# Kernel tuning notes

Hardware: AMD Instinct MI355X
Metric: run time of the kernel (lower is better)

The kernel has to match this reference:

```python
import jax, jax.numpy as jnp
import numpy as np

HEADS = 8
DIM_HEAD = 64
BN_EPS = 1e-5

def setup_inputs() -> dict:
    key = jax.random.key(0)
    ks = jax.random.split(key, 6)
    B, N, D = 8, 1024, 512
    inner = HEADS * DIM_HEAD  # 512
    return {
        "x": jax.random.normal(ks[0], (B, N, D), dtype=jnp.float32),
        "w_qkv": jax.random.normal(ks[1], (D, 3 * inner), dtype=jnp.float32) * (D ** -0.5),
        "conv_w": jax.random.normal(ks[2], (HEADS, HEADS), dtype=jnp.float32) * (HEADS ** -0.5),
        "conv_b": jax.random.normal(ks[3], (HEADS,), dtype=jnp.float32) * 0.02,
        "bn_gamma": jnp.ones((HEADS,), dtype=jnp.float32),
        "bn_beta": jnp.zeros((HEADS,), dtype=jnp.float32),
        "w_out": jax.random.normal(ks[4], (inner, D), dtype=jnp.float32) * (inner ** -0.5),
        "b_out": jnp.zeros((D,), dtype=jnp.float32),
    }

def reference(x, w_qkv, conv_w, conv_b, bn_gamma, bn_beta, w_out, b_out):
    B, N, D = x.shape
    H, dh = HEADS, DIM_HEAD
    scale = dh ** -0.5
    qkv = x @ w_qkv  # [B, N, 3*H*dh]
    q, k, v = jnp.split(qkv, 3, axis=-1)
    # b n (h d) -> b h n d
    q = q.reshape(B, N, H, dh).transpose(0, 2, 1, 3)
    k = k.reshape(B, N, H, dh).transpose(0, 2, 1, 3)
    v = v.reshape(B, N, H, dh).transpose(0, 2, 1, 3)
    attn = jnp.einsum('bhnd,bhmd->bhnm', q, k) * scale
    attn = jax.nn.softmax(attn, axis=-1)
    # 1x1 conv across heads (channels = heads)
    attn = jnp.einsum('gh,bhnm->bgnm', conv_w, attn) + conv_b[None, :, None, None]
    # BatchNorm2d in training mode: batch stats over (B, N, N) per head, biased variance
    mean = attn.mean(axis=(0, 2, 3), keepdims=True)
    var = attn.var(axis=(0, 2, 3), keepdims=True)
    attn = (attn - mean) * jax.lax.rsqrt(var + BN_EPS)
    attn = attn * bn_gamma[None, :, None, None] + bn_beta[None, :, None, None]
    # reatten_scale = 1.0 (transform_scale=False)
    out = jnp.einsum('bhnm,bhmd->bhnd', attn, v)
    out = out.transpose(0, 2, 1, 3).reshape(B, N, H * dh)  # b h n d -> b n (h d)
    return out @ w_out + b_out
```

## Files before the change

kernel.cpp:

```cpp
#include <hip/hip_runtime.h>
#include <math.h>


#define Bz 8
#define Nn 1024
#define Dd 512
#define Hh 8
#define DH 64
#define INNER 512
#define QW 1536
#define SCALE 0.125f
#define BN_EPS 1e-5f

typedef short bf16x8 __attribute__((ext_vector_type(8)));
typedef float f32x4 __attribute__((ext_vector_type(4)));

#define MFMA(a, b, c) __builtin_amdgcn_mfma_f32_16x16x32_bf16((a), (b), (c), 0, 0, 0)

__device__ __forceinline__ unsigned short f2b(float f) {
  union { float f; unsigned u; } v; v.f = f;
  unsigned r = v.u + 0x7fffu + ((v.u >> 16) & 1u);
  return (unsigned short)(r >> 16);
}
__device__ __forceinline__ float b2f(unsigned short s) {
  union { unsigned u; float f; } v; v.u = ((unsigned)s) << 16;
  return v.f;
}

#define WB_XB 0u
#define WB_QKV 8388608u
#define WB_O1A 0u
#define WB_O1B 16777216u
#define WB_VT 33554432u
#define WB_SG 41943040u
#define WB_O1BF WB_SG
#define WB_WQT 176160768u
#define WB_WOT 177733632u
#define WB_RSUM 178257920u
#define WB_VSUM 178520064u
#define WB_STATS 178536448u
#define WB_AC 178536512u

__global__ __launch_bounds__(256) void k_xbf(const float* __restrict__ X,
                                             unsigned short* __restrict__ XB) {
  const size_t i = ((size_t)blockIdx.x * 256 + threadIdx.x) * 8;
  float4 f0 = *(const float4*)(X + i);
  float4 f1 = *(const float4*)(X + i + 4);
  unsigned short o[8] = {f2b(f0.x), f2b(f0.y), f2b(f0.z), f2b(f0.w),
                         f2b(f1.x), f2b(f1.y), f2b(f1.z), f2b(f1.w)};
  *(uint4*)(XB + i) = *(uint4*)o;
}

__global__ __launch_bounds__(256) void k_transpose(const float* __restrict__ src,
                                                   unsigned short* __restrict__ dst,
                                                   int R, int C) {
  __shared__ float tile[32][33];
  const int tc = blockIdx.x * 32, tr = blockIdx.y * 32;
  const int lx = threadIdx.x & 31, ly = threadIdx.x >> 5;
#pragma unroll
  for (int i = 0; i < 32; i += 8)
    tile[ly + i][lx] = src[(size_t)(tr + ly + i) * C + tc + lx];
  __syncthreads();
#pragma unroll
  for (int i = 0; i < 32; i += 8)
    dst[(size_t)(tc + ly + i) * R + tr + lx] = f2b(tile[lx][ly + i]);
}

__global__ __launch_bounds__(256) void k_qkv(const unsigned short* __restrict__ XB,
                                             const unsigned short* __restrict__ WQT,
                                             unsigned short* __restrict__ qkv,
                                             unsigned short* __restrict__ vT) {
  extern __shared__ char smem[];
  unsigned short(*sA)[40] = (unsigned short(*)[40])smem;
  unsigned short(*sB)[40] = (unsigned short(*)[40])(smem + 128 * 40 * 2);
  unsigned short* sEp = (unsigned short*)smem;
  const int t = threadIdx.x;
  const int col0 = blockIdx.x * 128;
  const int row0 = blockIdx.y * 128;
  const bool isqk = (col0 < 2 * INNER);
  const int l = t & 63, w = t >> 6;
  const int wm = (w & 1) * 64, wn = (w >> 1) * 64;
  const int lm = l & 15, lq = l >> 4;
  const int srow = t >> 1, skc = (t & 1) * 16;
  f32x4 acc[4][4] = {};
  for (int k0 = 0; k0 < Dd; k0 += 32) {
    {
      const unsigned short* src = XB + (size_t)(row0 + srow) * Dd + k0 + skc;
      *(uint4*)&sA[srow][skc] = *(const uint4*)src;
      *(uint4*)&sA[srow][skc + 8] = *(const uint4*)(src + 8);
    }
    {
      const unsigned short* srcB = WQT + (size_t)(col0 + srow) * Dd + k0 + skc;
      *(uint4*)&sB[srow][skc] = *(const uint4*)srcB;
      *(uint4*)&sB[srow][skc + 8] = *(const uint4*)(srcB + 8);
    }
    __syncthreads();
    bf16x8 af[4], bfr[4];
#pragma unroll
    for (int i = 0; i < 4; i++) af[i] = *(const bf16x8*)&sA[wm + 16 * i + lm][lq * 8];
#pragma unroll
    for (int j = 0; j < 4; j++) bfr[j] = *(const bf16x8*)&sB[wn + 16 * j + lm][lq * 8];
    if (isqk) {
#pragma unroll
      for (int i = 0; i < 4; i++)
#pragma unroll
        for (int j = 0; j < 4; j++) acc[i][j] = MFMA(bfr[i], af[j], acc[i][j]);
    } else {
#pragma unroll
      for (int i = 0; i < 4; i++)
#pragma unroll
        for (int j = 0; j < 4; j++) acc[i][j] = MFMA(af[i], bfr[j], acc[i][j]);
    }
    __syncthreads();
  }
  if (isqk) {
#pragma unroll
    for (int jc = 0; jc < 4; jc++)
#pragma unroll
      for (int ir = 0; ir < 4; ir++) {
        unsigned short us[4];
#pragma unroll
        for (int r = 0; r < 4; r++) us[r] = f2b(acc[jc][ir][r]);
        *(uint2*)&sEp[(wm + 16 * ir + lm) * 136 + wn + 16 * jc + 4 * lq] = *(uint2*)us;
      }
    __syncthreads();
    const int row = t >> 1, half = t & 1;
    const unsigned short* src = &sEp[row * 136 + half * 64];
    unsigned short* dst = qkv + (size_t)(row0 + row) * QW + col0 + half * 64;
#pragma unroll
    for (int c = 0; c < 8; c++) *(uint4*)(dst + c * 8) = *(const uint4*)(src + c * 8);
  } else {
#pragma unroll
    for (int ir = 0; ir < 4; ir++)
#pragma unroll
      for (int jc = 0; jc < 4; jc++) {
        unsigned short us[4];
#pragma unroll
        for (int r = 0; r < 4; r++) us[r] = f2b(acc[ir][jc][r]);
        *(uint2*)&sEp[(wn + 16 * jc + lm) * 136 + wm + 16 * ir + 4 * lq] = *(uint2*)us;
      }
    __syncthreads();
    const int row = t >> 1, half = t & 1;
    const int gd = col0 - 2 * INNER + row;
    const int bq = row0 >> 10, mseq0 = row0 & 1023;
    const unsigned short* src = &sEp[row * 136 + half * 64];
    unsigned short* dst =
        vT + (((size_t)(bq * Hh + (gd >> 6)) * DH + (gd & 63)) << 10) + mseq0 + half * 64;
#pragma unroll
    for (int c = 0; c < 8; c++) *(uint4*)(dst + c * 8) = *(const uint4*)(src + c * 8);
  }
}

__global__ __launch_bounds__(256) void k_vsum(const unsigned short* __restrict__ vT,
                                              float* __restrict__ vsum) {
  const int bg = blockIdx.x;
  const int d = threadIdx.x >> 2, qq = threadIdx.x & 3;
  __shared__ float red[64][4];
  const unsigned short* p = vT + ((size_t)bg * DH + d) * Nn + qq * 256;
  float s = 0.f;
  for (int m = 0; m < 256; m += 4) {
    uint2 rr = *(const uint2*)(p + m);
    s += b2f((unsigned short)(rr.x & 0xffff)) + b2f((unsigned short)(rr.x >> 16)) +
         b2f((unsigned short)(rr.y & 0xffff)) + b2f((unsigned short)(rr.y >> 16));
  }
  red[d][qq] = s;
  __syncthreads();
  if (threadIdx.x < 64)
    vsum[(size_t)bg * DH + threadIdx.x] =
        red[threadIdx.x][0] + red[threadIdx.x][1] + red[threadIdx.x][2] + red[threadIdx.x][3];
}

__global__ __launch_bounds__(512, 4) void k_sgen(const unsigned short* __restrict__ qkv,
                                                 unsigned short* __restrict__ Sg,
                                                 float* __restrict__ rsum) {
  __shared__ unsigned short sK[8 * 32 * 72];
  __shared__ unsigned short sT[32 * 264];
  const int b = blockIdx.x;
  const int n0 = blockIdx.y * 32;
  const int mh = blockIdx.z;
  const int t = threadIdx.x;
  const int w = t >> 6, l = t & 63;
  const int lm = l & 15, lq = l >> 4;
  bf16x8 qf[2][2];
#pragma unroll
  for (int i = 0; i < 2; i++) {
    const unsigned short* qp =
        qkv + (size_t)(b * Nn + n0 + 16 * i + lm) * QW + w * DH + lq * 8;
    qf[i][0] = *(const bf16x8*)qp;
    qf[i][1] = *(const bf16x8*)(qp + 32);
  }
  float psum[2] = {0.f, 0.f};
  for (int it = 0; it < 16; it++) {
    const int m0 = mh * 512 + it * 32;
    {
#pragma unroll
      for (int s = 0; s < 4; s++) {
        const int c = t + s * 512;
        const int hh = c >> 8, mm = (c >> 3) & 31, qq = c & 7;
        *(uint4*)&sK[(hh * 32 + mm) * 72 + qq * 8] = *(const uint4*)(
            qkv + (size_t)(b * Nn + m0 + mm) * QW + INNER + hh * DH + qq * 8);
      }
    }
    __syncthreads();
    f32x4 lac[2][2] = {};
#pragma unroll
    for (int jm = 0; jm < 2; jm++) {
      bf16x8 ka0 = *(const bf16x8*)&sK[(w * 32 + 16 * jm + lm) * 72 + lq * 8];
      bf16x8 ka1 = *(const bf16x8*)&sK[(w * 32 + 16 * jm + lm) * 72 + 32 + lq * 8];
#pragma unroll
      for (int i = 0; i < 2; i++) {
        lac[i][jm] = MFMA(ka0, qf[i][0], lac[i][jm]);
        lac[i][jm] = MFMA(ka1, qf[i][1], lac[i][jm]);
      }
    }
#pragma unroll
    for (int i = 0; i < 2; i++)
#pragma unroll
      for (int jm = 0; jm < 2; jm++)
#pragma unroll
        for (int r = 0; r < 4; r++) {
          float e = __expf(lac[i][jm][r] * SCALE);
          psum[i] += e;
          sT[(16 * i + lm) * 264 + (16 * jm + 4 * lq + r) * 8 + w] = f2b(e);
        }
    __syncthreads();
    {
      const int row = t >> 4, ck = t & 15;
      unsigned short* dst =
          Sg + (((size_t)(b * Nn + n0 + row) << 10) + m0) * 8 + ck * 16;
      const unsigned short* src = &sT[row * 264 + ck * 16];
      *(uint4*)dst = *(const uint4*)src;
      *(uint4*)(dst + 8) = *(const uint4*)(src + 8);
    }
  }
#pragma unroll
  for (int i = 0; i < 2; i++) {
    psum[i] += __shfl_xor(psum[i], 16);
    psum[i] += __shfl_xor(psum[i], 32);
  }
  if (lq == 0) {
    atomicAdd(&rsum[(size_t)(b * Hh + w) * Nn + n0 + lm], psum[0]);
    atomicAdd(&rsum[(size_t)(b * Hh + w) * Nn + n0 + 16 + lm], psum[1]);
  }
}

__global__ __launch_bounds__(512, 4) void k_mixsv(const unsigned short* __restrict__ Sg,
                                                  const unsigned short* __restrict__ vT,
                                                  const float* __restrict__ rsum,
                                                  const float* __restrict__ conv_w,
                                                  float* __restrict__ O1A,
                                                  float* __restrict__ O1B,
                                                  float* __restrict__ stats) {
  __shared__ unsigned short sU[2][8][16][68];
  __shared__ float sRed[8][16];
  const int b = blockIdx.x;
  const int n0 = blockIdx.y * 16;
  const int mbase = blockIdx.z * 512;
  float* __restrict__ O1 = blockIdx.z ? O1B : O1A;
  const int t = threadIdx.x;
  const int w = t >> 6, l = t & 63;
  const int lm = l & 15, lq = l >> 4;
  const int mxn = t >> 5, mxm = (t & 31) * 2;
  float cw[64];
#pragma unroll
  for (int i = 0; i < 64; i++) cw[i] = conv_w[i];
  float rv[8];
#pragma unroll
  for (int h = 0; h < 8; h++) rv[h] = 1.0f / rsum[(size_t)(b * Hh + h) * Nn + n0 + mxn];
  const unsigned short* sN = Sg + ((size_t)(b * Nn + n0 + mxn) << 13);
  f32x4 oacc[4] = {};
  float su[8] = {}, su2[8] = {};
  uint4 sreg[2][2];
  {
    const unsigned short* p = sN + ((size_t)(mbase + mxm) << 3);
    sreg[0][0] = *(const uint4*)p;
    sreg[0][1] = *(const uint4*)(p + 8);
  }
#pragma unroll
  for (int it = 0; it < 8; it++) {
    const int cur = it & 1, nxt = cur ^ 1;
    if (it < 7) {
      const unsigned short* p = sN + ((size_t)(mbase + (it + 1) * 64 + mxm) << 3);
      sreg[nxt][0] = *(const uint4*)p;
      sreg[nxt][1] = *(const uint4*)(p + 8);
    }
    {
      float sx[8], sy[8];
      const unsigned* pe = (const unsigned*)&sreg[cur][0];
      const unsigned* po = (const unsigned*)&sreg[cur][1];
#pragma unroll
      for (int h = 0; h < 4; h++) {
        sx[2 * h] = b2f((unsigned short)(pe[h] & 0xffff)) * rv[2 * h];
        sx[2 * h + 1] = b2f((unsigned short)(pe[h] >> 16)) * rv[2 * h + 1];
        sy[2 * h] = b2f((unsigned short)(po[h] & 0xffff)) * rv[2 * h];
        sy[2 * h + 1] = b2f((unsigned short)(po[h] >> 16)) * rv[2 * h + 1];
      }
#pragma unroll
      for (int g = 0; g < 8; g++) {
        float u0 = 0.f, u1 = 0.f;
#pragma unroll
        for (int h = 0; h < 8; h++) {
          u0 += cw[g * 8 + h] * sx[h];
          u1 += cw[g * 8 + h] * sy[h];
        }
        su[g] += u0 + u1;
        su2[g] += u0 * u0 + u1 * u1;
        *(unsigned*)&sU[cur][g][mxn][mxm] = (unsigned)f2b(u0) | ((unsigned)f2b(u1) << 16);
      }
    }
    __syncthreads();
    {
      bf16x8 uf0 = *(const bf16x8*)&sU[cur][w][lm][lq * 8];
      bf16x8 uf1 = *(const bf16x8*)&sU[cur][w][lm][32 + lq * 8];
#pragma unroll
      for (int j = 0; j < 4; j++) {
        const unsigned short* vp =
            vT + (((size_t)(b * Hh + w) * DH + 16 * j + lm) << 10) + mbase + it * 64 + lq * 8;
        bf16x8 v0 = *(const bf16x8*)vp;
        bf16x8 v1 = *(const bf16x8*)(vp + 32);
        oacc[j] = MFMA(uf0, v0, oacc[j]);
        oacc[j] = MFMA(uf1, v1, oacc[j]);
      }
    }
  }
#pragma unroll
  for (int j = 0; j < 4; j++)
#pragma unroll
    for (int r = 0; r < 4; r++)
      O1[((size_t)(b * Hh + w) * Nn + n0 + lq * 4 + r) * DH + 16 * j + lm] = oacc[j][r];
#pragma unroll
  for (int g = 0; g < 8; g++) {
    float a = su[g], q = su2[g];
    for (int off = 32; off; off >>= 1) {
      a += __shfl_down(a, off);
      q += __shfl_down(q, off);
    }
    if (l == 0) {
      sRed[w][g] = a;
      sRed[w][8 + g] = q;
    }
  }
  __syncthreads();
  if (t < 16) {
    float s = 0.f;
#pragma unroll
    for (int ww = 0; ww < 8; ww++) s += sRed[ww][t];
    atomicAdd(&stats[t], s);
  }
}

__global__ void k_alpha(const float* __restrict__ stats, const float* __restrict__ bn_gamma,
                        const float* __restrict__ bn_beta, float* __restrict__ ac) {
  const int g = threadIdx.x;
  if (g < 8) {
    const float cnt = (float)Bz * (float)Nn * (float)Nn;
    float Eu = stats[g] / cnt;
    float Eu2 = stats[8 + g] / cnt;
    float inv = rsqrtf(Eu2 - Eu * Eu + BN_EPS);
    float alpha = bn_gamma[g] * inv;
    ac[g] = alpha;
    ac[8 + g] = bn_beta[g] - Eu * alpha;
  }
}

__global__ __launch_bounds__(256) void k_o1aff(const float* __restrict__ O1A,
                                               const float* __restrict__ O1B,
                                               const float* __restrict__ vsum,
                                               const float* __restrict__ ac,
                                               unsigned short* __restrict__ O1BF) {
  const size_t i4 = ((size_t)blockIdx.x * 256 + threadIdx.x) * 4;
  const int bg = (int)(i4 >> 16);
  const int g = bg & 7;
  const int d = (int)(i4 & 63);
  float4 a = *(const float4*)(O1A + i4);
  float4 bb = *(const float4*)(O1B + i4);
  float4 v = *(const float4*)(vsum + (size_t)bg * DH + d);
  const float al = ac[g], cc = ac[8 + g];
  unsigned short o[4] = {f2b(al * (a.x + bb.x) + cc * v.x), f2b(al * (a.y + bb.y) + cc * v.y),
                         f2b(al * (a.z + bb.z) + cc * v.z), f2b(al * (a.w + bb.w) + cc * v.w)};
  *(uint2*)(O1BF + i4) = *(uint2*)o;
}

__global__ __launch_bounds__(256) void k_out(const unsigned short* __restrict__ O1BF,
                                             const unsigned short* __restrict__ WOT,
                                             const float* __restrict__ bout,
                                             float* __restrict__ out) {
  __shared__ unsigned short sA[128][40];
  __shared__ unsigned short sB[128][40];
  const int t = threadIdx.x;
  const int col0 = blockIdx.x * 128, row0 = blockIdx.y * 128;
  const int l = t & 63, w = t >> 6;
  const int wm = (w & 1) * 64, wn = (w >> 1) * 64;
  const int lm = l & 15, lq = l >> 4;
  const int srow = t >> 1, skc = (t & 1) * 16;
  const int b = row0 >> 10;
  const int nn = (row0 + srow) & 1023;
  f32x4 acc[4][4] = {};
  for (int k0 = 0; k0 < INNER; k0 += 32) {
    {
      const int k = k0 + skc;
      const int g = k >> 6, dd = k & 63;
      const unsigned short* src = O1BF + ((size_t)(b * Hh + g) * Nn + nn) * DH + dd;
      *(uint4*)&sA[srow][skc] = *(const uint4*)src;
      *(uint4*)&sA[srow][skc + 8] = *(const uint4*)(src + 8);
    }
    {
      const unsigned short* srcB = WOT + (size_t)(col0 + srow) * INNER + k0 + skc;
      *(uint4*)&sB[srow][skc] = *(const uint4*)srcB;
      *(uint4*)&sB[srow][skc + 8] = *(const uint4*)(srcB + 8);
    }
    __syncthreads();
    bf16x8 af[4], bfr[4];
#pragma unroll
    for (int i = 0; i < 4; i++) af[i] = *(const bf16x8*)&sA[wm + 16 * i + lm][lq * 8];
#pragma unroll
    for (int j = 0; j < 4; j++) bfr[j] = *(const bf16x8*)&sB[wn + 16 * j + lm][lq * 8];
#pragma unroll
    for (int i = 0; i < 4; i++)
#pragma unroll
      for (int j = 0; j < 4; j++) acc[i][j] = MFMA(af[i], bfr[j], acc[i][j]);
    __syncthreads();
  }
#pragma unroll
  for (int j = 0; j < 4; j++) {
    const int col = col0 + wn + 16 * j + lm;
    const float bo = bout[col];
#pragma unroll
    for (int i = 0; i < 4; i++) {
      const int rbase = row0 + wm + 16 * i + lq * 4;
#pragma unroll
      for (int r = 0; r < 4; r++) out[(size_t)(rbase + r) * Dd + col] = acc[i][j][r] + bo;
    }
  }
}

extern "C" void kernel_launch(void* const* d_in, const int* in_sizes, int n_in,
                              void* d_out, int out_size, void* d_ws, size_t ws_size,
                              hipStream_t stream) {
  const float* x = (const float*)d_in[0];
  const float* w_qkv = (const float*)d_in[1];
  const float* conv_w = (const float*)d_in[2];
  const float* bn_gamma = (const float*)d_in[4];
  const float* bn_beta = (const float*)d_in[5];
  const float* w_out = (const float*)d_in[6];
  const float* b_out = (const float*)d_in[7];
  char* ws = (char*)d_ws;
  unsigned short* XB = (unsigned short*)(ws + WB_XB);
  unsigned short* QKV = (unsigned short*)(ws + WB_QKV);
  unsigned short* VT = (unsigned short*)(ws + WB_VT);
  unsigned short* SG = (unsigned short*)(ws + WB_SG);
  unsigned short* WQT = (unsigned short*)(ws + WB_WQT);
  unsigned short* WOT = (unsigned short*)(ws + WB_WOT);
  float* O1Ap = (float*)(ws + WB_O1A);
  float* O1Bp = (float*)(ws + WB_O1B);
  unsigned short* O1BF = (unsigned short*)(ws + WB_O1BF);
  float* RSUM = (float*)(ws + WB_RSUM);
  float* VSUM = (float*)(ws + WB_VSUM);
  float* STATS = (float*)(ws + WB_STATS);
  float* AC = (float*)(ws + WB_AC);

  hipMemsetAsync(STATS, 0, 64, stream);
  hipMemsetAsync(RSUM, 0, 262144, stream);
  k_xbf<<<2048, 256, 0, stream>>>(x, XB);
  k_transpose<<<dim3(48, 16), 256, 0, stream>>>(w_qkv, WQT, 512, 1536);
  k_transpose<<<dim3(16, 16), 256, 0, stream>>>(w_out, WOT, 512, 512);
  k_qkv<<<dim3(12, 64), 256, 34816, stream>>>(XB, WQT, QKV, VT);
  k_vsum<<<64, 256, 0, stream>>>(VT, VSUM);
  k_sgen<<<dim3(8, 32, 2), 512, 0, stream>>>(QKV, SG, RSUM);
  k_mixsv<<<dim3(8, 64, 2), 512, 0, stream>>>(SG, VT, RSUM, conv_w, O1Ap, O1Bp, STATS);
  k_alpha<<<1, 64, 0, stream>>>(STATS, bn_gamma, bn_beta, AC);
  k_o1aff<<<4096, 256, 0, stream>>>(O1Ap, O1Bp, VSUM, AC, O1BF);
  k_out<<<dim3(4, 64), 256, 0, stream>>>(O1BF, WOT, b_out, (float*)d_out);
}
```

Baseline: 328.4 us.

## Switch bf16 to fp16 MFMA and merge split-M mixsv into one pass

```diff
diff --git a/kernel.cpp b/kernel.cpp
--- a/kernel.cpp
+++ b/kernel.cpp
@@ -12,25 +12,26 @@
 #define SCALE 0.125f
 #define BN_EPS 1e-5f
 
-typedef short bf16x8 __attribute__((ext_vector_type(8)));
+typedef _Float16 __f16;
+typedef __f16 f16x8 __attribute__((ext_vector_type(8)));
 typedef float f32x4 __attribute__((ext_vector_type(4)));
 
-#define MFMA(a, b, c) __builtin_amdgcn_mfma_f32_16x16x32_bf16((a), (b), (c), 0, 0, 0)
-
-__device__ __forceinline__ unsigned short f2b(float f) {
-  union { float f; unsigned u; } v; v.f = f;
-  unsigned r = v.u + 0x7fffu + ((v.u >> 16) & 1u);
-  return (unsigned short)(r >> 16);
-}
-__device__ __forceinline__ float b2f(unsigned short s) {
-  union { unsigned u; float f; } v; v.u = ((unsigned)s) << 16;
-  return v.f;
+#define MFMA16(a, b, c) __builtin_amdgcn_mfma_f32_16x16x32_f16((a), (b), (c), 0, 0, 0)
+
+__device__ __forceinline__ unsigned short f2h(float f) {
+  union { __f16 h; unsigned short s; } v;
+  v.h = (__f16)f;
+  return v.s;
+}
+__device__ __forceinline__ float h2f(unsigned short s) {
+  union { unsigned short s; __f16 h; } v;
+  v.s = s;
+  return (float)v.h;
 }
 
 #define WB_XB 0u
 #define WB_QKV 8388608u
-#define WB_O1A 0u
-#define WB_O1B 16777216u
+#define WB_O1 0u
 #define WB_VT 33554432u
 #define WB_SG 41943040u
 #define WB_O1BF WB_SG
@@ -46,8 +47,8 @@
   const size_t i = ((size_t)blockIdx.x * 256 + threadIdx.x) * 8;
   float4 f0 = *(const float4*)(X + i);
   float4 f1 = *(const float4*)(X + i + 4);
-  unsigned short o[8] = {f2b(f0.x), f2b(f0.y), f2b(f0.z), f2b(f0.w),
-                         f2b(f1.x), f2b(f1.y), f2b(f1.z), f2b(f1.w)};
+  unsigned short o[8] = {f2h(f0.x), f2h(f0.y), f2h(f0.z), f2h(f0.w),
+                         f2h(f1.x), f2h(f1.y), f2h(f1.z), f2h(f1.w)};
   *(uint4*)(XB + i) = *(uint4*)o;
 }
 
@@ -63,7 +64,7 @@
   __syncthreads();
 #pragma unroll
   for (int i = 0; i < 32; i += 8)
-    dst[(size_t)(tc + ly + i) * R + tr + lx] = f2b(tile[lx][ly + i]);
+    dst[(size_t)(tc + ly + i) * R + tr + lx] = f2h(tile[lx][ly + i]);
 }
 
 __global__ __launch_bounds__(256) void k_qkv(const unsigned short* __restrict__ XB,
@@ -95,21 +96,21 @@
       *(uint4*)&sB[srow][skc + 8] = *(const uint4*)(srcB + 8);
     }
     __syncthreads();
-    bf16x8 af[4], bfr[4];
-#pragma unroll
-    for (int i = 0; i < 4; i++) af[i] = *(const bf16x8*)&sA[wm + 16 * i + lm][lq * 8];
-#pragma unroll
-    for (int j = 0; j < 4; j++) bfr[j] = *(const bf16x8*)&sB[wn + 16 * j + lm][lq * 8];
+    f16x8 af[4], bfr[4];
+#pragma unroll
+    for (int i = 0; i < 4; i++) af[i] = *(const f16x8*)&sA[wm + 16 * i + lm][lq * 8];
+#pragma unroll
+    for (int j = 0; j < 4; j++) bfr[j] = *(const f16x8*)&sB[wn + 16 * j + lm][lq * 8];
     if (isqk) {
 #pragma unroll
       for (int i = 0; i < 4; i++)
 #pragma unroll
-        for (int j = 0; j < 4; j++) acc[i][j] = MFMA(bfr[i], af[j], acc[i][j]);
+        for (int j = 0; j < 4; j++) acc[i][j] = MFMA16(bfr[i], af[j], acc[i][j]);
     } else {
 #pragma unroll
       for (int i = 0; i < 4; i++)
 #pragma unroll
-        for (int j = 0; j < 4; j++) acc[i][j] = MFMA(af[i], bfr[j], acc[i][j]);
+        for (int j = 0; j < 4; j++) acc[i][j] = MFMA16(af[i], bfr[j], acc[i][j]);
     }
     __syncthreads();
   }
@@ -120,7 +121,7 @@
       for (int ir = 0; ir < 4; ir++) {
         unsigned short us[4];
 #pragma unroll
-        for (int r = 0; r < 4; r++) us[r] = f2b(acc[jc][ir][r]);
+        for (int r = 0; r < 4; r++) us[r] = f2h(acc[jc][ir][r]);
         *(uint2*)&sEp[(wm + 16 * ir + lm) * 136 + wn + 16 * jc + 4 * lq] = *(uint2*)us;
       }
     __syncthreads();
@@ -136,7 +137,7 @@
       for (int jc = 0; jc < 4; jc++) {
         unsigned short us[4];
 #pragma unroll
-        for (int r = 0; r < 4; r++) us[r] = f2b(acc[ir][jc][r]);
+        for (int r = 0; r < 4; r++) us[r] = f2h(acc[ir][jc][r]);
         *(uint2*)&sEp[(wn + 16 * jc + lm) * 136 + wm + 16 * ir + 4 * lq] = *(uint2*)us;
       }
     __syncthreads();
@@ -160,8 +161,8 @@
   float s = 0.f;
   for (int m = 0; m < 256; m += 4) {
     uint2 rr = *(const uint2*)(p + m);
-    s += b2f((unsigned short)(rr.x & 0xffff)) + b2f((unsigned short)(rr.x >> 16)) +
-         b2f((unsigned short)(rr.y & 0xffff)) + b2f((unsigned short)(rr.y >> 16));
+    s += h2f((unsigned short)(rr.x & 0xffff)) + h2f((unsigned short)(rr.x >> 16)) +
+         h2f((unsigned short)(rr.y & 0xffff)) + h2f((unsigned short)(rr.y >> 16));
   }
   red[d][qq] = s;
   __syncthreads();
@@ -170,7 +171,7 @@
         red[threadIdx.x][0] + red[threadIdx.x][1] + red[threadIdx.x][2] + red[threadIdx.x][3];
 }
 
-__global__ __launch_bounds__(512, 4) void k_sgen(const unsigned short* __restrict__ qkv,
+__global__ __launch_bounds__(512, 2) void k_sgen(const unsigned short* __restrict__ qkv,
                                                  unsigned short* __restrict__ Sg,
                                                  float* __restrict__ rsum) {
   __shared__ unsigned short sK[8 * 32 * 72];
@@ -181,13 +182,13 @@
   const int t = threadIdx.x;
   const int w = t >> 6, l = t & 63;
   const int lm = l & 15, lq = l >> 4;
-  bf16x8 qf[2][2];
+  f16x8 qf[2][2];
 #pragma unroll
   for (int i = 0; i < 2; i++) {
     const unsigned short* qp =
         qkv + (size_t)(b * Nn + n0 + 16 * i + lm) * QW + w * DH + lq * 8;
-    qf[i][0] = *(const bf16x8*)qp;
-    qf[i][1] = *(const bf16x8*)(qp + 32);
+    qf[i][0] = *(const f16x8*)qp;
+    qf[i][1] = *(const f16x8*)(qp + 32);
   }
   float psum[2] = {0.f, 0.f};
   for (int it = 0; it < 16; it++) {
@@ -205,12 +206,12 @@
     f32x4 lac[2][2] = {};
 #pragma unroll
     for (int jm = 0; jm < 2; jm++) {
-      bf16x8 ka0 = *(const bf16x8*)&sK[(w * 32 + 16 * jm + lm) * 72 + lq * 8];
-      bf16x8 ka1 = *(const bf16x8*)&sK[(w * 32 + 16 * jm + lm) * 72 + 32 + lq * 8];
+      f16x8 ka0 = *(const f16x8*)&sK[(w * 32 + 16 * jm + lm) * 72 + lq * 8];
+      f16x8 ka1 = *(const f16x8*)&sK[(w * 32 + 16 * jm + lm) * 72 + 32 + lq * 8];
 #pragma unroll
       for (int i = 0; i < 2; i++) {
-        lac[i][jm] = MFMA(ka0, qf[i][0], lac[i][jm]);
-        lac[i][jm] = MFMA(ka1, qf[i][1], lac[i][jm]);
+        lac[i][jm] = MFMA16(ka0, qf[i][0], lac[i][jm]);
+        lac[i][jm] = MFMA16(ka1, qf[i][1], lac[i][jm]);
       }
     }
 #pragma unroll
@@ -221,7 +222,7 @@
         for (int r = 0; r < 4; r++) {
           float e = __expf(lac[i][jm][r] * SCALE);
           psum[i] += e;
-          sT[(16 * i + lm) * 264 + (16 * jm + 4 * lq + r) * 8 + w] = f2b(e);
+          sT[(16 * i + lm) * 264 + (16 * jm + 4 * lq + r) * 8 + w] = f2h(e);
         }
     __syncthreads();
     {
@@ -244,19 +245,16 @@
   }
 }
 
-__global__ __launch_bounds__(512, 4) void k_mixsv(const unsigned short* __restrict__ Sg,
+__global__ __launch_bounds__(512, 2) void k_mixsv(const unsigned short* __restrict__ Sg,
                                                   const unsigned short* __restrict__ vT,
                                                   const float* __restrict__ rsum,
                                                   const float* __restrict__ conv_w,
-                                                  float* __restrict__ O1A,
-                                                  float* __restrict__ O1B,
+                                                  float* __restrict__ O1,
                                                   float* __restrict__ stats) {
-  __shared__ unsigned short sU[2][8][16][68];
+  __shared__ unsigned short sU[8][16][68];
   __shared__ float sRed[8][16];
   const int b = blockIdx.x;
   const int n0 = blockIdx.y * 16;
-  const int mbase = blockIdx.z * 512;
-  float* __restrict__ O1 = blockIdx.z ? O1B : O1A;
   const int t = threadIdx.x;
   const int w = t >> 6, l = t & 63;
   const int lm = l & 15, lq = l >> 4;
@@ -267,33 +265,32 @@
   float rv[8];
 #pragma unroll
   for (int h = 0; h < 8; h++) rv[h] = 1.0f / rsum[(size_t)(b * Hh + h) * Nn + n0 + mxn];
-  const unsigned short* sN = Sg + ((size_t)(b * Nn + n0 + mxn) << 13);
+  const unsigned short* sNp = Sg + ((size_t)(b * Nn + n0 + mxn) << 13);
   f32x4 oacc[4] = {};
   float su[8] = {}, su2[8] = {};
-  uint4 sreg[2][2];
+  uint4 c0, c1;
   {
-    const unsigned short* p = sN + ((size_t)(mbase + mxm) << 3);
-    sreg[0][0] = *(const uint4*)p;
-    sreg[0][1] = *(const uint4*)(p + 8);
-  }
-#pragma unroll
-  for (int it = 0; it < 8; it++) {
-    const int cur = it & 1, nxt = cur ^ 1;
-    if (it < 7) {
-      const unsigned short* p = sN + ((size_t)(mbase + (it + 1) * 64 + mxm) << 3);
-      sreg[nxt][0] = *(const uint4*)p;
-      sreg[nxt][1] = *(const uint4*)(p + 8);
-    }
-    {
+    const unsigned short* p = sNp + (mxm << 3);
+    c0 = *(const uint4*)p;
+    c1 = *(const uint4*)(p + 8);
+  }
+  for (int it = 0; it < 16; it++) {
+    uint4 nx0, nx1;
+    if (it < 15) {
+      const unsigned short* p = sNp + ((size_t)((it + 1) * 64 + mxm) << 3);
+      nx0 = *(const uint4*)p;
+      nx1 = *(const uint4*)(p + 8);
+    }
+    {
+      const unsigned* pe = (const unsigned*)&c0;
+      const unsigned* po = (const unsigned*)&c1;
       float sx[8], sy[8];
-      const unsigned* pe = (const unsigned*)&sreg[cur][0];
-      const unsigned* po = (const unsigned*)&sreg[cur][1];
-#pragma unroll
-      for (int h = 0; h < 4; h++) {
-        sx[2 * h] = b2f((unsigned short)(pe[h] & 0xffff)) * rv[2 * h];
-        sx[2 * h + 1] = b2f((unsigned short)(pe[h] >> 16)) * rv[2 * h + 1];
-        sy[2 * h] = b2f((unsigned short)(po[h] & 0xffff)) * rv[2 * h];
-        sy[2 * h + 1] = b2f((unsigned short)(po[h] >> 16)) * rv[2 * h + 1];
+#pragma unroll
+      for (int hp = 0; hp < 4; hp++) {
+        sx[2 * hp] = h2f((unsigned short)(pe[hp] & 0xffff)) * rv[2 * hp];
+        sx[2 * hp + 1] = h2f((unsigned short)(pe[hp] >> 16)) * rv[2 * hp + 1];
+        sy[2 * hp] = h2f((unsigned short)(po[hp] & 0xffff)) * rv[2 * hp];
+        sy[2 * hp + 1] = h2f((unsigned short)(po[hp] >> 16)) * rv[2 * hp + 1];
       }
 #pragma unroll
       for (int g = 0; g < 8; g++) {
@@ -305,22 +302,27 @@
         }
         su[g] += u0 + u1;
         su2[g] += u0 * u0 + u1 * u1;
-        *(unsigned*)&sU[cur][g][mxn][mxm] = (unsigned)f2b(u0) | ((unsigned)f2b(u1) << 16);
-      }
-    }
-    __syncthreads();
-    {
-      bf16x8 uf0 = *(const bf16x8*)&sU[cur][w][lm][lq * 8];
-      bf16x8 uf1 = *(const bf16x8*)&sU[cur][w][lm][32 + lq * 8];
+        *(unsigned*)&sU[g][mxn][mxm] = (unsigned)f2h(u0) | ((unsigned)f2h(u1) << 16);
+      }
+    }
+    __syncthreads();
+    {
+      f16x8 uf0 = *(const f16x8*)&sU[w][lm][lq * 8];
+      f16x8 uf1 = *(const f16x8*)&sU[w][lm][32 + lq * 8];
 #pragma unroll
       for (int j = 0; j < 4; j++) {
         const unsigned short* vp =
-            vT + (((size_t)(b * Hh + w) * DH + 16 * j + lm) << 10) + mbase + it * 64 + lq * 8;
-        bf16x8 v0 = *(const bf16x8*)vp;
-        bf16x8 v1 = *(const bf16x8*)(vp + 32);
-        oacc[j] = MFMA(uf0, v0, oacc[j]);
-        oacc[j] = MFMA(uf1, v1, oacc[j]);
-      }
+            vT + (((size_t)(b * Hh + w) * DH + 16 * j + lm) << 10) + it * 64 + lq * 8;
+        f16x8 v0 = *(const f16x8*)vp;
+        f16x8 v1 = *(const f16x8*)(vp + 32);
+        oacc[j] = MFMA16(uf0, v0, oacc[j]);
+        oacc[j] = MFMA16(uf1, v1, oacc[j]);
+      }
+    }
+    __syncthreads();
+    if (it < 15) {
+      c0 = nx0;
+      c1 = nx1;
     }
   }
 #pragma unroll
@@ -363,8 +365,7 @@
   }
 }
 
-__global__ __launch_bounds__(256) void k_o1aff(const float* __restrict__ O1A,
-                                               const float* __restrict__ O1B,
+__global__ __launch_bounds__(256) void k_o1aff(const float* __restrict__ O1,
                                                const float* __restrict__ vsum,
                                                const float* __restrict__ ac,
                                                unsigned short* __restrict__ O1BF) {
@@ -372,12 +373,11 @@
   const int bg = (int)(i4 >> 16);
   const int g = bg & 7;
   const int d = (int)(i4 & 63);
-  float4 a = *(const float4*)(O1A + i4);
-  float4 bb = *(const float4*)(O1B + i4);
+  float4 a = *(const float4*)(O1 + i4);
   float4 v = *(const float4*)(vsum + (size_t)bg * DH + d);
   const float al = ac[g], cc = ac[8 + g];
-  unsigned short o[4] = {f2b(al * (a.x + bb.x) + cc * v.x), f2b(al * (a.y + bb.y) + cc * v.y),
-                         f2b(al * (a.z + bb.z) + cc * v.z), f2b(al * (a.w + bb.w) + cc * v.w)};
+  unsigned short o[4] = {f2h(al * a.x + cc * v.x), f2h(al * a.y + cc * v.y),
+                         f2h(al * a.z + cc * v.z), f2h(al * a.w + cc * v.w)};
   *(uint2*)(O1BF + i4) = *(uint2*)o;
 }
 
@@ -410,15 +410,15 @@
       *(uint4*)&sB[srow][skc + 8] = *(const uint4*)(srcB + 8);
     }
     __syncthreads();
-    bf16x8 af[4], bfr[4];
-#pragma unroll
-    for (int i = 0; i < 4; i++) af[i] = *(const bf16x8*)&sA[wm + 16 * i + lm][lq * 8];
-#pragma unroll
-    for (int j = 0; j < 4; j++) bfr[j] = *(const bf16x8*)&sB[wn + 16 * j + lm][lq * 8];
+    f16x8 af[4], bfr[4];
+#pragma unroll
+    for (int i = 0; i < 4; i++) af[i] = *(const f16x8*)&sA[wm + 16 * i + lm][lq * 8];
+#pragma unroll
+    for (int j = 0; j < 4; j++) bfr[j] = *(const f16x8*)&sB[wn + 16 * j + lm][lq * 8];
 #pragma unroll
     for (int i = 0; i < 4; i++)
 #pragma unroll
-      for (int j = 0; j < 4; j++) acc[i][j] = MFMA(af[i], bfr[j], acc[i][j]);
+      for (int j = 0; j < 4; j++) acc[i][j] = MFMA16(af[i], bfr[j], acc[i][j]);
     __syncthreads();
   }
 #pragma unroll
@@ -451,8 +451,7 @@
   unsigned short* SG = (unsigned short*)(ws + WB_SG);
   unsigned short* WQT = (unsigned short*)(ws + WB_WQT);
   unsigned short* WOT = (unsigned short*)(ws + WB_WOT);
-  float* O1Ap = (float*)(ws + WB_O1A);
-  float* O1Bp = (float*)(ws + WB_O1B);
+  float* O1 = (float*)(ws + WB_O1);
   unsigned short* O1BF = (unsigned short*)(ws + WB_O1BF);
   float* RSUM = (float*)(ws + WB_RSUM);
   float* VSUM = (float*)(ws + WB_VSUM);
@@ -467,8 +466,8 @@
   k_qkv<<<dim3(12, 64), 256, 34816, stream>>>(XB, WQT, QKV, VT);
   k_vsum<<<64, 256, 0, stream>>>(VT, VSUM);
   k_sgen<<<dim3(8, 32, 2), 512, 0, stream>>>(QKV, SG, RSUM);
-  k_mixsv<<<dim3(8, 64, 2), 512, 0, stream>>>(SG, VT, RSUM, conv_w, O1Ap, O1Bp, STATS);
+  k_mixsv<<<dim3(8, 64), 512, 0, stream>>>(SG, VT, RSUM, conv_w, O1, STATS);
   k_alpha<<<1, 64, 0, stream>>>(STATS, bn_gamma, bn_beta, AC);
-  k_o1aff<<<4096, 256, 0, stream>>>(O1Ap, O1Bp, VSUM, AC, O1BF);
+  k_o1aff<<<4096, 256, 0, stream>>>(O1, VSUM, AC, O1BF);
   k_out<<<dim3(4, 64), 256, 0, stream>>>(O1BF, WOT, b_out, (float*)d_out);
 }
```

Measured after the change: 271.7 us. 17.3% less time.
